# Kernel optimization log

Hardware: AMD Instinct MI355X
Metric: run time of the kernel (lower is better)

Reference implementation:

```python
import jax, jax.numpy as jnp
import numpy as np

N = 50000      # num nodes
E = 800000     # num edges (avg degree 16)
IN, H, OUT = 128, 128, 16
R = 8          # num relations


def rgcn_conv(x, edge_index, edge_type, W, root, bias, num_relations):
    """PyG RGCNConv with aggr='mean': out = x@root + bias + sum_r mean_{j in N_r(i)} x_j @ W_r.
    Mean is linear, so aggregate raw x_j per relation first, then one matmul per relation."""
    src, dst = edge_index[0], edge_index[1]  # messages flow src -> dst
    x_src = x[src]                            # [E, F] gather
    out = x @ root + bias                     # root/self term
    for r in range(num_relations):            # small fixed loop over relations
        m = (edge_type == r).astype(x.dtype)  # [E]
        s = jax.ops.segment_sum(x_src * m[:, None], dst, num_segments=x.shape[0])  # [N, F]
        c = jax.ops.segment_sum(m, dst, num_segments=x.shape[0])                   # [N]
        out = out + (s / jnp.maximum(c, 1.0)[:, None]) @ W[r]
    return out


def setup_inputs() -> dict:
    key = jax.random.key(0)
    ks = jax.random.split(key, 12)
    glorot = lambda k, shape: jax.random.normal(k, shape, jnp.float32) * (2.0 / (shape[-2] + shape[-1])) ** 0.5
    return {
        "x": jax.random.normal(ks[0], (N, IN), jnp.float32),
        "edge_index": jax.random.randint(ks[1], (2, E), 0, N, jnp.int64) if jax.config.read('jax_enable_x64') else jax.random.randint(ks[1], (2, E), 0, N).astype(jnp.int32),
        "edge_type": jax.random.randint(ks[2], (E,), 0, R).astype(jnp.int32),
        "w0": glorot(ks[3], (R, IN, H)),
        "root0": glorot(ks[4], (IN, H)),
        "b0": jnp.zeros((H,), jnp.float32),
        "w1": glorot(ks[5], (R, H, H)),
        "root1": glorot(ks[6], (H, H)),
        "b1": jnp.zeros((H,), jnp.float32),
        "w2": glorot(ks[7], (R, H, OUT)),
        "root2": glorot(ks[8], (H, OUT)),
        "b2": jnp.zeros((OUT,), jnp.float32),
    }


def reference(x, edge_index, edge_type, w0, root0, b0, w1, root1, b1, w2, root2, b2):
    # layer 0: in -> hidden, relu (dropout is identity in eval mode)
    h = jax.nn.relu(rgcn_conv(x, edge_index, edge_type, w0, root0, b0, R))
    # layer 1: hidden -> hidden, relu
    h = jax.nn.relu(rgcn_conv(h, edge_index, edge_type, w1, root1, b1, R))
    # layer 2: hidden -> out (no activation)
    return rgcn_conv(h, edge_index, edge_type, w2, root2, b2, R)
```

## Files before the change

### kernel.cpp

```cpp
#include <hip/hip_runtime.h>

#define N_NODES 50000
#define N_EDGES 800000
#define NREL 8
#define NB8 (N_NODES * NREL)
#define SCAN_T 12500
#define KSTEPS 36
#define A_STRIDE 1160
#define NT32 1563

typedef __attribute__((ext_vector_type(8))) short short8;
typedef __attribute__((ext_vector_type(4))) float f32x4;
typedef __attribute__((ext_vector_type(2))) float f32x2;

__device__ __forceinline__ unsigned short f2bf(float v) {
    union { float f; unsigned int u; } c; c.f = v;
    return (unsigned short)((c.u + 0x7FFFu + ((c.u >> 16) & 1u)) >> 16);
}
__device__ __forceinline__ float bfhi2f(unsigned int u) {
    union { unsigned int u; float f; } c; c.u = u & 0xFFFF0000u; return c.f;
}
__device__ __forceinline__ float bflo2f(unsigned int u) {
    union { unsigned int u; float f; } c; c.u = u << 16; return c.f;
}

#define PREP_Z   (NB8 / 4)
#define PREP_X   (N_NODES * 32)
#define PREP_P   (8 * KSTEPS * 64)
#define PREP_P2  (1 * KSTEPS * 64)
#define PREP_TOTAL (PREP_Z + PREP_X + 2 * PREP_P + PREP_P2)

__device__ __forceinline__ void pack_one(int idx, const float* __restrict__ root,
                                         const float* __restrict__ W,
                                         unsigned short* __restrict__ Wpack, int FOUT) {
    int lane = idx & 63;
    int ks = (idx >> 6) % KSTEPS;
    int ct = idx / (KSTEPS * 64);
    int kbase = ks * 32 + (lane >> 4) * 8;
    int col = ct * 16 + (lane & 15);
    union { unsigned short us[8]; uint4 v; } u;
#pragma unroll
    for (int j = 0; j < 8; j++) {
        int k = kbase + j;
        float val = (k < 128) ? root[(size_t)k * FOUT + col]
                              : W[(size_t)(k - 128) * FOUT + col];
        u.us[j] = f2bf(val);
    }
    ((uint4*)Wpack)[idx] = u.v;
}

__global__ void prep_kernel(const float* __restrict__ X, unsigned int* __restrict__ Xb2,
                            const float* __restrict__ r0, const float* __restrict__ w0,
                            unsigned short* __restrict__ Wp0,
                            const float* __restrict__ r1, const float* __restrict__ w1,
                            unsigned short* __restrict__ Wp1,
                            const float* __restrict__ r2, const float* __restrict__ w2,
                            unsigned short* __restrict__ Wp2,
                            int* __restrict__ cnt) {
    int t = blockIdx.x * blockDim.x + threadIdx.x;
    if (t < PREP_Z) { ((int4*)cnt)[t] = make_int4(0, 0, 0, 0); return; }
    t -= PREP_Z;
    if (t < PREP_X) {
        float4 v = ((const float4*)X)[t];
        unsigned int p0 = (unsigned int)f2bf(v.x) | ((unsigned int)f2bf(v.y) << 16);
        unsigned int p1 = (unsigned int)f2bf(v.z) | ((unsigned int)f2bf(v.w) << 16);
        ((uint2*)Xb2)[t] = make_uint2(p0, p1);
        return;
    }
    t -= PREP_X;
    if (t < PREP_P) { pack_one(t, r0, w0, Wp0, 128); return; }
    t -= PREP_P;
    if (t < PREP_P) { pack_one(t, r1, w1, Wp1, 128); return; }
    t -= PREP_P;
    if (t < PREP_P2) pack_one(t, r2, w2, Wp2, 16);
}

__global__ void rank_kernel(const int* __restrict__ ei, const int* __restrict__ et,
                            int* __restrict__ cnt, int* __restrict__ rank, int E) {
    int e = blockIdx.x * blockDim.x + threadIdx.x;
    if (e >= E) return;
    int d = ei[E + e];
    int t = et[e];
    rank[e] = atomicAdd(&cnt[d * NREL + t], 1);
}

__global__ void scanA_kernel(const int* __restrict__ cnt, int* __restrict__ tsum) {
    int g = blockIdx.x * blockDim.x + threadIdx.x;
    if (g >= SCAN_T) return;
    const int4* p = (const int4*)(cnt + (size_t)g * 32);
    int s = 0;
#pragma unroll
    for (int j = 0; j < 8; j++) {
        int4 v = p[j];
        s += v.x + v.y + v.z + v.w;
    }
    tsum[g] = s;
}

__global__ void scanB_kernel(const int* __restrict__ tsum, int* __restrict__ toff) {
    __shared__ int part[1024];
    int t = threadIdx.x;
    const int C = 13;
    int n0 = t * C, n1 = n0 + C; if (n1 > SCAN_T) n1 = SCAN_T;
    int s = 0;
    for (int n = n0; n < n1; n++) s += tsum[n];
    part[t] = s;
    __syncthreads();
    for (int off = 1; off < 1024; off <<= 1) {
        int v = (t >= off) ? part[t - off] : 0;
        __syncthreads();
        part[t] += v;
        __syncthreads();
    }
    int run = (t > 0) ? part[t - 1] : 0;
    for (int n = n0; n < n1; n++) { toff[n] = run; run += tsum[n]; }
}

__global__ void scanC_kernel(const int* __restrict__ cnt, const int* __restrict__ toff,
                             int* __restrict__ rs8) {
    int g = blockIdx.x * blockDim.x + threadIdx.x;
    if (g >= SCAN_T) return;
    int run = toff[g];
    int base = g * 32;
#pragma unroll 4
    for (int j = 0; j < 32; j++) {
        rs8[base + j] = run;
        run += cnt[base + j];
    }
    if (g == 0) rs8[NB8] = N_EDGES;
}

__global__ void place_kernel(const int* __restrict__ ei, const int* __restrict__ et,
                             const int* __restrict__ rank, const int* __restrict__ rs8,
                             unsigned short* __restrict__ csr_src, int E) {
    int e = blockIdx.x * blockDim.x + threadIdx.x;
    if (e >= E) return;
    int s = ei[e];
    int d = ei[E + e];
    int t = et[e];
    csr_src[rs8[d * NREL + t] + rank[e]] = (unsigned short)s;
}

template <int FOUT, bool RELU>
__global__ __launch_bounds__(1024, 8) void layer_kernel(
    const unsigned int* __restrict__ Xb2,
    const int* __restrict__ rs8,
    const unsigned short* __restrict__ csr_src,
    const unsigned short* __restrict__ Wpack,
    const float* __restrict__ bias,
    void* __restrict__ Yout)
{
    __shared__ __align__(16) unsigned short Abuf[32][A_STRIDE];

    int tid = threadIdx.x;
    int wave = tid >> 6, lane = tid & 63;
    int l15 = lane & 15;
    int node0 = blockIdx.x * 32;

    int gn0 = node0 + wave * 2;
    if (gn0 < N_NODES) {
        unsigned int* row0 = (unsigned int*)&Abuf[wave * 2][0];
        unsigned int* row1 = (unsigned int*)&Abuf[wave * 2 + 1][0];

        int bl = lane <= 16 ? lane : 16;
        int bv = rs8[gn0 * 8 + bl];
        unsigned int self0 = Xb2[(size_t)gn0 * 64 + lane];
        unsigned int self1 = Xb2[(size_t)(gn0 + 1) * 64 + lane];

        int e     = __builtin_amdgcn_readlane(bv, 0);
        int e_end = __builtin_amdgcn_readlane(bv, 16);

        row0[lane] = self0;
        row1[lane] = self1;

        int r = 0;
        int segs = e;
        int be = __builtin_amdgcn_readlane(bv, 1);
        f32x2 av = (f32x2){0.f, 0.f};

#define FLUSH_R()                                                              \
        do {                                                                   \
            int c_ = be - segs;                                                \
            float iv_ = __builtin_amdgcn_rcpf((float)(c_ > 0 ? c_ : 1));       \
            unsigned int pk_;                                                  \
            asm("v_cvt_pk_bf16_f32 %0, %1, %2"                                 \
                : "=v"(pk_) : "v"(av.x * iv_), "v"(av.y * iv_));               \
            unsigned int* rw_ = (r < 8) ? row0 : row1;                         \
            rw_[(1 + (r & 7)) * 64 + lane] = pk_;                              \
            av = (f32x2){0.f, 0.f}; segs = be; r++;                            \
            be = __builtin_amdgcn_readlane(bv, r + 1 <= 16 ? r + 1 : 16);      \
        } while (0)

        if (e < e_end) {
            int e1m = e_end - 1;
            int ma = e + l15; if (ma > e1m) ma = e1m;
            unsigned int mv = csr_src[ma];
            while (e < e_end) {
                int bn = e_end - e; if (bn > 16) bn = 16;
                int sc[16];
#pragma unroll
                for (int k = 0; k < 16; k++) sc[k] = __builtin_amdgcn_readlane((int)mv, k);
                unsigned int xp[16];
#pragma unroll
                for (int k = 0; k < 16; k++) xp[k] = Xb2[(size_t)sc[k] * 64 + lane];
                int en = e + bn;
                if (en < e_end) {
                    int mb = en + l15; if (mb > e1m) mb = e1m;
                    mv = csr_src[mb];
                }
#pragma unroll
                for (int k = 0; k < 16; k++) {
                    if (k < bn) {
                        int ec = e + k;
                        while (ec >= be) FLUSH_R();
                        av += (f32x2){bflo2f(xp[k]), bfhi2f(xp[k])};
                    }
                }
                e = en;
            }
        }
        while (r < 16) FLUSH_R();
#undef FLUSH_R
    }
    __syncthreads();

    int quad = lane >> 4, l16 = lane & 15;
    int swz = lane & 7;
    if constexpr (FOUT == 128) {
        int ct = wave & 7, kh = wave >> 3;
        f32x4 acc0 = (f32x4){0.f, 0.f, 0.f, 0.f};
        f32x4 acc1 = (f32x4){0.f, 0.f, 0.f, 0.f};
        int ks0 = kh * 18;
        for (int ks = ks0; ks < ks0 + 18; ks++) {
            short8 b = *(const short8*)(Wpack + (((size_t)ct * KSTEPS + ks) * 64 + lane) * 8);
            short8 a0 = *(const short8*)&Abuf[l16][ks * 32 + quad * 8];
            short8 a1 = *(const short8*)&Abuf[16 + l16][ks * 32 + quad * 8];
            acc0 = __builtin_amdgcn_mfma_f32_16x16x32_bf16(a0, b, acc0, 0, 0, 0);
            acc1 = __builtin_amdgcn_mfma_f32_16x16x32_bf16(a1, b, acc1, 0, 0, 0);
        }
        __syncthreads();
        f32x4* rv = (f32x4*)&Abuf[0][0];
        if (wave >= 8) {
            int sb = ((wave - 8) * 64 + lane) * 2;
            rv[sb ^ swz]       = acc0;
            rv[(sb + 1) ^ swz] = acc1;
        }
        __syncthreads();
        if (wave < 8) {
            int sb = (wave * 64 + lane) * 2;
            f32x4 s0 = acc0 + rv[sb ^ swz];
            f32x4 s1 = acc1 + rv[(sb + 1) ^ swz];
            unsigned short* Yb = (unsigned short*)Yout;
            int h = ct * 16 + l16;
            float bvs = bias[h];
#pragma unroll
            for (int r4 = 0; r4 < 4; r4++) {
                int n0r = node0 + quad * 4 + r4;
                float v0 = s0[r4] + bvs;
                if (RELU) v0 = v0 > 0.f ? v0 : 0.f;
                Yb[(size_t)n0r * 128 + h] = f2bf(v0);
                int n1r = node0 + 16 + quad * 4 + r4;
                float v1 = s1[r4] + bvs;
                if (RELU) v1 = v1 > 0.f ? v1 : 0.f;
                if (n1r < N_NODES) Yb[(size_t)n1r * 128 + h] = f2bf(v1);
            }
        }
    } else {
        int ks0 = (wave < 4) ? wave * 3 : 12 + (wave - 4) * 2;
        int ksn = (wave < 4) ? 3 : 2;
        f32x4 acc0 = (f32x4){0.f, 0.f, 0.f, 0.f};
        f32x4 acc1 = (f32x4){0.f, 0.f, 0.f, 0.f};
        for (int ks = ks0; ks < ks0 + ksn; ks++) {
            short8 b = *(const short8*)(Wpack + ((size_t)ks * 64 + lane) * 8);
            short8 a0 = *(const short8*)&Abuf[l16][ks * 32 + quad * 8];
            short8 a1 = *(const short8*)&Abuf[16 + l16][ks * 32 + quad * 8];
            acc0 = __builtin_amdgcn_mfma_f32_16x16x32_bf16(a0, b, acc0, 0, 0, 0);
            acc1 = __builtin_amdgcn_mfma_f32_16x16x32_bf16(a1, b, acc1, 0, 0, 0);
        }
        __syncthreads();
        float* red = (float*)&Abuf[0][0];
        f32x4* rv = (f32x4*)red;
        int sb = (wave * 64 + lane) * 2;
        rv[sb ^ swz]       = acc0;
        rv[(sb + 1) ^ swz] = acc1;
        __syncthreads();
        if (tid < 512) {
            int nr = tid >> 4, h = tid & 15;
            int g = nr >> 4, rem = nr & 15;
            int q_ = rem >> 2, r4 = rem & 3;
            int lsrc = q_ * 16 + h;
            float s = 0.f;
#pragma unroll
            for (int w2 = 0; w2 < 16; w2++) {
                int sl = ((w2 * 64 + lsrc) * 2 + g) ^ (lsrc & 7);
                s += red[sl * 4 + r4];
            }
            int node = node0 + nr;
            float v = s + bias[h];
            if (RELU) v = v > 0.f ? v : 0.f;
            if (node < N_NODES)
                ((float*)Yout)[(size_t)node * 16 + h] = v;
        }
    }
}

extern "C" void kernel_launch(void* const* d_in, const int* in_sizes, int n_in,
                              void* d_out, int out_size, void* d_ws, size_t ws_size,
                              hipStream_t stream) {
    const float* x  = (const float*)d_in[0];
    const int*   ei = (const int*)d_in[1];
    const int*   et = (const int*)d_in[2];
    const float* w0 = (const float*)d_in[3];
    const float* r0 = (const float*)d_in[4];
    const float* b0 = (const float*)d_in[5];
    const float* w1 = (const float*)d_in[6];
    const float* r1 = (const float*)d_in[7];
    const float* b1 = (const float*)d_in[8];
    const float* w2 = (const float*)d_in[9];
    const float* r2 = (const float*)d_in[10];
    const float* b2 = (const float*)d_in[11];

    char* wsp = (char*)d_ws;
    size_t off = 0;
    auto alloc = [&](size_t bytes) -> void* {
        void* p = wsp + off;
        off += (bytes + 255) & ~(size_t)255;
        return p;
    };

    int* cnt    = (int*)alloc((size_t)NB8 * 4);
    int* rs8    = (int*)alloc(((size_t)NB8 + 1) * 4);
    int* rank   = (int*)alloc((size_t)N_EDGES * 4);
    int* tsum   = (int*)alloc((size_t)SCAN_T * 4);
    int* toff   = (int*)alloc((size_t)SCAN_T * 4);
    unsigned short* csr_src = (unsigned short*)alloc((size_t)N_EDGES * 2);
    unsigned short* Wp0 = (unsigned short*)alloc((size_t)8 * KSTEPS * 64 * 8 * 2);
    unsigned short* Wp1 = (unsigned short*)alloc((size_t)8 * KSTEPS * 64 * 8 * 2);
    unsigned short* Wp2 = (unsigned short*)alloc((size_t)1 * KSTEPS * 64 * 8 * 2);
    unsigned int* Xb = (unsigned int*)alloc((size_t)N_NODES * 64 * 4);
    unsigned int* H0 = (unsigned int*)alloc((size_t)N_NODES * 64 * 4);
    unsigned int* H1 = (unsigned int*)alloc((size_t)N_NODES * 64 * 4);

    prep_kernel<<<dim3((PREP_TOTAL + 255) / 256), dim3(256), 0, stream>>>(
        x, Xb, r0, w0, Wp0, r1, w1, Wp1, r2, w2, Wp2, cnt);
    rank_kernel<<<dim3((N_EDGES + 255) / 256), dim3(256), 0, stream>>>(ei, et, cnt, rank, N_EDGES);
    scanA_kernel<<<dim3((SCAN_T + 255) / 256), dim3(256), 0, stream>>>(cnt, tsum);
    scanB_kernel<<<dim3(1), dim3(1024), 0, stream>>>(tsum, toff);
    scanC_kernel<<<dim3((SCAN_T + 255) / 256), dim3(256), 0, stream>>>(cnt, toff, rs8);
    place_kernel<<<dim3((N_EDGES + 255) / 256), dim3(256), 0, stream>>>(ei, et, rank, rs8,
                                                                        csr_src, N_EDGES);

    layer_kernel<128, true ><<<dim3(NT32), dim3(1024), 0, stream>>>(
        Xb, rs8, csr_src, Wp0, b0, (void*)H0);
    layer_kernel<128, true ><<<dim3(NT32), dim3(1024), 0, stream>>>(
        H0, rs8, csr_src, Wp1, b1, (void*)H1);
    layer_kernel<16, false><<<dim3(NT32), dim3(1024), 0, stream>>>(
        H1, rs8, csr_src, Wp2, b2, d_out);
}
```

Baseline: 291.1 us.

## Double-buffer neighbor gathers, widen index prefetch, pack-add accumulation, raise MFMA priority

Restructures the per-wave edge aggregation loop so the gather of the next 16 neighbor rows is issued before the current 16 are accumulated, using two register buffers. Source indices are now loaded 64 at a time (one per lane) and refilled every four windows. Accumulation uses an explicit v_pk_add_f32, and the MFMA loops run with raised wave priority. The goal is to hide gather latency behind accumulation, at the cost of higher register pressure and possible lower occupancy.

```diff
diff --git a/kernel.cpp b/kernel.cpp
--- a/kernel.cpp
+++ b/kernel.cpp
@@ -22,6 +22,16 @@
 }
 __device__ __forceinline__ float bflo2f(unsigned int u) {
     union { unsigned int u; float f; } c; c.u = u << 16; return c.f;
+}
+__device__ __forceinline__ void pk_acc(f32x2& av, unsigned int u) {
+    f32x2 x;
+    x.x = bflo2f(u);
+    x.y = bfhi2f(u);
+    unsigned long long a, b;
+    __builtin_memcpy(&a, &av, 8);
+    __builtin_memcpy(&b, &x, 8);
+    asm("v_pk_add_f32 %0, %1, %2" : "=v"(a) : "v"(a), "v"(b));
+    __builtin_memcpy(&av, &a, 8);
 }
 
 #define PREP_Z   (NB8 / 4)
@@ -167,14 +177,14 @@
         unsigned int self0 = Xb2[(size_t)gn0 * 64 + lane];
         unsigned int self1 = Xb2[(size_t)(gn0 + 1) * 64 + lane];
 
-        int e     = __builtin_amdgcn_readlane(bv, 0);
+        int e0    = __builtin_amdgcn_readlane(bv, 0);
         int e_end = __builtin_amdgcn_readlane(bv, 16);
 
         row0[lane] = self0;
         row1[lane] = self1;
 
         int r = 0;
-        int segs = e;
+        int segs = e0;
         int be = __builtin_amdgcn_readlane(bv, 1);
         f32x2 av = (f32x2){0.f, 0.f};
 
@@ -191,33 +201,60 @@
             be = __builtin_amdgcn_readlane(bv, r + 1 <= 16 ? r + 1 : 16);      \
         } while (0)
 
-        if (e < e_end) {
+        if (e0 < e_end) {
             int e1m = e_end - 1;
-            int ma = e + l15; if (ma > e1m) ma = e1m;
-            unsigned int mv = csr_src[ma];
-            while (e < e_end) {
-                int bn = e_end - e; if (bn > 16) bn = 16;
-                int sc[16];
-#pragma unroll
-                for (int k = 0; k < 16; k++) sc[k] = __builtin_amdgcn_readlane((int)mv, k);
-                unsigned int xp[16];
-#pragma unroll
-                for (int k = 0; k < 16; k++) xp[k] = Xb2[(size_t)sc[k] * 64 + lane];
-                int en = e + bn;
-                if (en < e_end) {
-                    int mb = en + l15; if (mb > e1m) mb = e1m;
-                    mv = csr_src[mb];
-                }
-#pragma unroll
-                for (int k = 0; k < 16; k++) {
-                    if (k < bn) {
-                        int ec = e + k;
-                        while (ec >= be) FLUSH_R();
-                        av += (f32x2){bflo2f(xp[k]), bfhi2f(xp[k])};
-                    }
-                }
-                e = en;
+            int nw = (e_end - e0 + 15) >> 4;
+            int ml = e0 + lane; if (ml > e1m) ml = e1m;
+            unsigned int mv = csr_src[ml];
+
+            unsigned int xpA[16], xpB[16];
+
+#define ISSUE_W(XP, WI)                                                        \
+            do {                                                               \
+                int mb_ = ((WI) & 3) << 4;                                     \
+                _Pragma("unroll")                                              \
+                for (int k = 0; k < 16; k++) {                                 \
+                    int s_ = __builtin_amdgcn_readlane((int)mv, mb_ + k);      \
+                    XP[k] = Xb2[(size_t)s_ * 64 + lane];                       \
+                }                                                              \
+            } while (0)
+
+#define REFILL_M(WI)                                                           \
+            do {                                                               \
+                if (((WI) & 3) == 0 && (WI) > 0) {                             \
+                    int mb_ = e0 + (((WI) >> 2) << 6) + lane;                  \
+                    if (mb_ > e1m) mb_ = e1m;                                  \
+                    mv = csr_src[mb_];                                         \
+                }                                                              \
+            } while (0)
+
+#define ACCUM_W(XP, WI)                                                        \
+            do {                                                               \
+                int ws_ = e0 + ((WI) << 4);                                    \
+                int bn_ = e_end - ws_; if (bn_ > 16) bn_ = 16;                 \
+                _Pragma("unroll")                                              \
+                for (int k = 0; k < 16; k++) {                                 \
+                    if (k < bn_) {                                             \
+                        int ec = ws_ + k;                                      \
+                        while (ec >= be) FLUSH_R();                            \
+                        pk_acc(av, XP[k]);                                     \
+                    }                                                          \
+                }                                                              \
+            } while (0)
+
+            ISSUE_W(xpA, 0);
+            int i = 0;
+            for (;;) {
+                if (i + 1 < nw) { REFILL_M(i + 1); ISSUE_W(xpB, i + 1); }
+                ACCUM_W(xpA, i);
+                if (++i >= nw) break;
+                if (i + 1 < nw) { REFILL_M(i + 1); ISSUE_W(xpA, i + 1); }
+                ACCUM_W(xpB, i);
+                if (++i >= nw) break;
             }
+#undef ISSUE_W
+#undef REFILL_M
+#undef ACCUM_W
         }
         while (r < 16) FLUSH_R();
 #undef FLUSH_R
@@ -231,6 +268,7 @@
         f32x4 acc0 = (f32x4){0.f, 0.f, 0.f, 0.f};
         f32x4 acc1 = (f32x4){0.f, 0.f, 0.f, 0.f};
         int ks0 = kh * 18;
+        __builtin_amdgcn_s_setprio(1);
         for (int ks = ks0; ks < ks0 + 18; ks++) {
             short8 b = *(const short8*)(Wpack + (((size_t)ct * KSTEPS + ks) * 64 + lane) * 8);
             short8 a0 = *(const short8*)&Abuf[l16][ks * 32 + quad * 8];
@@ -238,6 +276,7 @@
             acc0 = __builtin_amdgcn_mfma_f32_16x16x32_bf16(a0, b, acc0, 0, 0, 0);
             acc1 = __builtin_amdgcn_mfma_f32_16x16x32_bf16(a1, b, acc1, 0, 0, 0);
         }
+        __builtin_amdgcn_s_setprio(0);
         __syncthreads();
         f32x4* rv = (f32x4*)&Abuf[0][0];
         if (wave >= 8) {
@@ -270,6 +309,7 @@
         int ksn = (wave < 4) ? 3 : 2;
         f32x4 acc0 = (f32x4){0.f, 0.f, 0.f, 0.f};
         f32x4 acc1 = (f32x4){0.f, 0.f, 0.f, 0.f};
+        __builtin_amdgcn_s_setprio(1);
         for (int ks = ks0; ks < ks0 + ksn; ks++) {
             short8 b = *(const short8*)(Wpack + ((size_t)ks * 64 + lane) * 8);
             short8 a0 = *(const short8*)&Abuf[l16][ks * 32 + quad * 8];
@@ -277,6 +317,7 @@
             acc0 = __builtin_amdgcn_mfma_f32_16x16x32_bf16(a0, b, acc0, 0, 0, 0);
             acc1 = __builtin_amdgcn_mfma_f32_16x16x32_bf16(a1, b, acc1, 0, 0, 0);
         }
+        __builtin_amdgcn_s_setprio(0);
         __syncthreads();
         float* red = (float*)&Abuf[0][0];
         f32x4* rv = (f32x4*)red;
```

Result: slower. 306.9 us (+5.4%).
